# Performance work log

Measured on AMD Instinct MI355X. Metric: run time of the kernel, lower is better.

Reference implementation:

```python
import jax, jax.numpy as jnp
import numpy as np

B, L, D_INNER, D_STATE, DT_RANK, MODES = 4, 2048, 256, 16, 16, 32
LN_EPS = 1e-5


def setup_inputs() -> dict:
    key = jax.random.key(0)
    ks = jax.random.split(key, 10)
    x = jax.random.normal(ks[0], (B, L, D_INNER), dtype=jnp.float32)
    ln_g = jnp.ones((D_INNER,), jnp.float32)
    ln_b = jnp.zeros((D_INNER,), jnp.float32)
    W_xproj = jax.random.normal(ks[1], (DT_RANK + 2 * D_STATE, D_INNER), jnp.float32) * (D_INNER ** -0.5)
    dt_init_std = DT_RANK ** -0.5  # dt_scale = 1.0
    W_dt = jax.random.uniform(ks[2], (D_INNER, DT_RANK), jnp.float32, -dt_init_std, dt_init_std)
    dt = jnp.exp(jax.random.uniform(ks[3], (D_INNER,), jnp.float32) * (np.log(0.1) - np.log(0.001)) + np.log(0.001))
    dt = jnp.clip(dt, 1e-4, None)
    b_dt = dt + jnp.log(-jnp.expm1(-dt))  # inverse softplus
    A_log = jnp.zeros((D_INNER, D_STATE), jnp.float32)  # log(ones)
    D_param = jnp.ones((D_INNER,), jnp.float32)
    scale = 1.0 / (D_STATE * D_STATE)
    w_re = scale * jax.random.uniform(ks[4], (D_STATE, D_STATE, MODES), jnp.float32)
    w_im = scale * jax.random.uniform(ks[5], (D_STATE, D_STATE, MODES), jnp.float32)
    return {"x": x, "ln_g": ln_g, "ln_b": ln_b, "W_xproj": W_xproj, "W_dt": W_dt,
            "b_dt": b_dt, "A_log": A_log, "D_param": D_param, "w_re": w_re, "w_im": w_im}


def _fft_kernel(hs, w_re, w_im):
    # hs: (B, L, d_inner, d_state); rfft over d_inner with d_state channels
    h = jnp.transpose(hs, (0, 1, 3, 2))  # (B, L, k, N)
    hf = jnp.fft.rfft(h, axis=-1)        # (B, L, k, N//2+1) complex
    n_freq = D_INNER // 2 + 1
    l = min(MODES, n_freq)
    w = (w_re + 1j * w_im).astype(hf.dtype)
    of = jnp.einsum('blix,iox->blox', hf[..., :l], w[..., :l])
    of = jnp.pad(of, ((0, 0), (0, 0), (0, 0), (0, n_freq - l)))
    h2 = jnp.fft.irfft(of, n=D_INNER, axis=-1)  # real, (B, L, k, N)
    return jnp.transpose(h2, (0, 1, 3, 2))      # (B, L, d_inner, d_state)


def reference(x, ln_g, ln_b, W_xproj, W_dt, b_dt, A_log, D_param, w_re, w_im):
    # LayerNorm
    mu = jnp.mean(x, axis=-1, keepdims=True)
    var = jnp.var(x, axis=-1, keepdims=True)
    xn = (x - mu) * jax.lax.rsqrt(var + LN_EPS) * ln_g + ln_b

    A = -jnp.exp(A_log)  # (d_inner, d_state)
    dbc = xn @ W_xproj.T  # (B, L, dt_rank + 2*d_state)
    delta_r = dbc[..., :DT_RANK]
    Bc = dbc[..., DT_RANK:DT_RANK + D_STATE]        # (B, L, d_state)
    Cc = dbc[..., DT_RANK + D_STATE:]               # (B, L, d_state)
    delta = jax.nn.softplus(delta_r @ W_dt.T + b_dt)  # (B, L, d_inner)

    deltaA = jnp.exp(delta[..., None] * A)                       # (B, L, d_inner, d_state)
    BX = delta[..., None] * Bc[:, :, None, :] * xn[..., None]    # (B, L, d_inner, d_state)

    # selective scan: h_t = deltaA_t * h_{t-1} + BX_t (parallel associative scan over L)
    def comb(c1, c2):
        a1, b1 = c1
        a2, b2 = c2
        return a1 * a2, a2 * b1 + b2
    _, hs = jax.lax.associative_scan(comb, (deltaA, BX), axis=1)

    hs = _fft_kernel(hs, w_re, w_im)
    y = jnp.einsum('bldn,bln->bld', hs, Cc)  # hs @ C
    y = y + D_param * xn
    return y + x
```

## Files before the change

### kernel.cpp

```cpp
#include <hip/hip_runtime.h>
#include <hip/hip_bf16.h>

#define B_   4
#define L_   2048
#define D_   256
#define NC   128
#define CL   16
#define NBLK (B_*NC)
#define ANG  0.02454369260617025967f

typedef __bf16 bf16x8 __attribute__((ext_vector_type(8)));
typedef __bf16 bf16x4 __attribute__((ext_vector_type(4)));
typedef float  f32x4  __attribute__((ext_vector_type(4)));

__global__ __launch_bounds__(256) void k_lnscan(
        const float* __restrict__ x, const float* __restrict__ ln_g, const float* __restrict__ ln_b,
        const float* __restrict__ W_xproj, const float* __restrict__ W_dt,
        const float* __restrict__ b_dt, const float* __restrict__ A_log,
        unsigned int* __restrict__ dxn,
        float* __restrict__ Bc_o, float* __restrict__ Cc_o,
        float* __restrict__ dsum_o, float* __restrict__ S)
{
    __shared__ __align__(16) float xn_s[16 * 260];
    __shared__ __align__(16) __bf16 xnb[16 * 256];
    __shared__ float dbc_s[16 * 52];
    int tid = threadIdx.x, wave = tid >> 6, lane = tid & 63;
    int blk = blockIdx.x;
    int grow0 = blk * CL;
    char* xnb_c = (char*)xnb;

#pragma unroll
    for (int rr = 0; rr < 4; rr++) {
        int r = wave * 4 + rr;
        const float* xr = x + (size_t)(grow0 + r) * D_;
        float v[4];
#pragma unroll
        for (int q = 0; q < 4; q++) v[q] = xr[lane + q * 64];
        float sum = v[0] + v[1] + v[2] + v[3];
        float sq  = v[0]*v[0] + v[1]*v[1] + v[2]*v[2] + v[3]*v[3];
#pragma unroll
        for (int off = 32; off; off >>= 1) { sum += __shfl_xor(sum, off); sq += __shfl_xor(sq, off); }
        float mu = sum * (1.f / D_);
        float rstd = rsqrtf(sq * (1.f / D_) - mu * mu + 1e-5f);
#pragma unroll
        for (int q = 0; q < 4; q++) {
            int d = lane + q * 64;
            float xv = (v[q] - mu) * rstd * ln_g[d] + ln_b[d];
            xn_s[r * 260 + d] = xv;
            *(__bf16*)(xnb_c + r * 512 + ((d * 2) ^ ((r & 7) << 4))) = (__bf16)xv;
        }
    }
    __syncthreads();

    if (wave < 3) {
        int jcol = wave * 16 + (lane & 15);
        const float* wrow = W_xproj + (size_t)jcol * 256 + ((lane >> 4) * 8);
        int mrow = lane & 15;
        f32x4 acc = {0.f, 0.f, 0.f, 0.f};
#pragma unroll
        for (int ks = 0; ks < 8; ks++) {
            bf16x8 af = *(const bf16x8*)(xnb_c + mrow * 512 +
                          ((ks * 64 + ((lane >> 4) * 16)) ^ ((mrow & 7) << 4)));
            f32x4 wa = *(const f32x4*)(wrow + ks * 32);
            f32x4 wb = *(const f32x4*)(wrow + ks * 32 + 4);
            bf16x8 bf;
#pragma unroll
            for (int k = 0; k < 4; k++) { bf[k] = (__bf16)wa[k]; bf[4 + k] = (__bf16)wb[k]; }
            acc = __builtin_amdgcn_mfma_f32_16x16x32_bf16(af, bf, acc, 0, 0, 0);
        }
#pragma unroll
        for (int q = 0; q < 4; q++) {
            int r = (lane >> 4) * 4 + q;
            dbc_s[r * 52 + jcol] = acc[q];
            if (jcol >= 32)      Cc_o[(size_t)(grow0 + r) * 16 + jcol - 32] = acc[q];
            else if (jcol >= 16) Bc_o[(size_t)(grow0 + r) * 16 + jcol - 16] = acc[q];
        }
    }
    __syncthreads();

    int d = tid;
    float wdt[16];
#pragma unroll
    for (int q = 0; q < 4; q++) {
        f32x4 w4 = *(const f32x4*)&W_dt[d * 16 + q * 4];
#pragma unroll
        for (int k = 0; k < 4; k++) wdt[q * 4 + k] = w4[k];
    }
    float bd = b_dt[d];
    float dlt_r[16];
#pragma unroll
    for (int r = 0; r < 16; r++) {
        float din = bd;
#pragma unroll
        for (int k = 0; k < 16; k++) din = fmaf(dbc_s[r * 52 + k], wdt[k], din);
        din = (din > 15.f) ? din : log1pf(__expf(din));
        dlt_r[r] = din;
        union { __bf16 h2[2]; unsigned int u; } pk;
        pk.h2[0] = (__bf16)din;
        pk.h2[1] = (__bf16)xn_s[r * 260 + d];
        dxn[(size_t)(grow0 + r) * D_ + d] = pk.u;
    }

    float ar[16];
#pragma unroll
    for (int q = 0; q < 4; q++) {
        f32x4 a4 = *(const f32x4*)&A_log[d * 16 + q * 4];
#pragma unroll
        for (int k = 0; k < 4; k++) ar[q * 4 + k] = -__expf(a4[k]);
    }
    bool uni = true;
#pragma unroll
    for (int n = 1; n < 16; n++) uni = uni && (ar[n] == ar[0]);
    float s[16], dsum = 0.f;
#pragma unroll
    for (int n = 0; n < 16; n++) s[n] = 0.f;
    if (uni) {
        float ar0 = ar[0];
#pragma unroll
        for (int t = 0; t < CL; t++) {
            float dl = dlt_r[t];
            float dx = dl * xn_s[t * 260 + d];
            dsum += dl;
            float e = __expf(dl * ar0);
#pragma unroll
            for (int n = 0; n < 16; n++)
                s[n] = fmaf(e, s[n], dx * dbc_s[t * 52 + 16 + n]);
        }
    } else {
#pragma unroll
        for (int t = 0; t < CL; t++) {
            float dl = dlt_r[t];
            float dx = dl * xn_s[t * 260 + d];
            dsum += dl;
#pragma unroll
            for (int n = 0; n < 16; n++) {
                float e = __expf(dl * ar[n]);
                s[n] = fmaf(e, s[n], dx * dbc_s[t * 52 + 16 + n]);
            }
        }
    }
    dsum_o[(size_t)blk * 256 + d] = dsum;
    size_t o = (size_t)blk * 4096 + d * 16;
#pragma unroll
    for (int q = 0; q < 4; q++) {
        f32x4 sv;
#pragma unroll
        for (int k = 0; k < 4; k++) sv[k] = s[q*4+k];
        *reinterpret_cast<f32x4*>(&S[o + q * 4]) = sv;
    }
}

__global__ __launch_bounds__(256) void k_scan_tab(
        const float* __restrict__ A_log, const float* __restrict__ dsum,
        float* __restrict__ S_H0,
        const float* __restrict__ w_re, const float* __restrict__ w_im,
        __hip_bfloat16* __restrict__ E_t, __hip_bfloat16* __restrict__ wfrag,
        __hip_bfloat16* __restrict__ E_inv)
{
    int blk = blockIdx.x;
    if (blk >= NBLK) {
        int idx = (blk - NBLK) * 256 + threadIdx.x;
        if (idx < 16384) {
            int x = idx >> 8, d = idx & 255;
            float v = (x < 32) ? __cosf(ANG * (float)((x * d) & 255))
                               : -__sinf(ANG * (float)(((x - 32) * d) & 255));
            E_t[idx] = __float2bfloat16(v);
        } else if (idx < 49152) {
            int f = idx - 16384;
            int nt = f >> 9, l = (f >> 3) & 63, j = f & 7;
            int n = nt * 16 + (l & 15);
            int o = ((l >> 4) & 3) * 8 + j;
            float v = 0.f;
            if (o < 16) {
                int comp = n >> 9, xm = (n >> 4) & 31, i = n & 15;
                v = comp ? w_im[(i * 16 + o) * 32 + xm] : w_re[(i * 16 + o) * 32 + xm];
            }
            wfrag[f] = __float2bfloat16(v);
        } else {
            int f = idx - 49152;
            int nt = f >> 10, ks = (f >> 9) & 1, l = (f >> 3) & 63, j = f & 7;
            int row = ks * 32 + ((l >> 4) & 3) * 8 + j;
            int col = nt * 16 + (l & 15);
            float v = (row < 32) ? __cosf(ANG * (float)((row * col) & 255))
                                 : -__sinf(ANG * (float)(((row - 32) * col) & 255));
            E_inv[f] = __float2bfloat16(v);
        }
        return;
    }
    __shared__ float gP[256];
    __shared__ float gS[256];
    int tid = threadIdx.x;
    int g2 = tid >> 5, cl2 = tid & 31;
    int ch = blk * 32 + cl2;
    int b2 = ch >> 12, dn2 = ch & 4095;
    int dd = dn2 >> 4;
    float arv = -__expf(A_log[dn2]);
    size_t cb = ((size_t)b2 * NC + g2 * 16) * 4096 + dn2;
    size_t db = ((size_t)b2 * NC + g2 * 16) * 256 + dd;
    float pv[16], sv[16];
#pragma unroll
    for (int c = 0; c < 16; c++) {
        pv[c] = __expf(arv * dsum[db + (size_t)c * 256]);
        sv[c] = S_H0[cb + (size_t)c * 4096];
    }
    float pA = 1.f, sA = 0.f;
#pragma unroll
    for (int c = 0; c < 16; c++) { sA = fmaf(pv[c], sA, sv[c]); pA *= pv[c]; }
    gP[g2 * 32 + cl2] = pA;
    gS[g2 * 32 + cl2] = sA;
    __syncthreads();
    float h = 0.f;
    for (int gg = 0; gg < g2; gg++)
        h = fmaf(gP[gg * 32 + cl2], h, gS[gg * 32 + cl2]);
#pragma unroll
    for (int c = 0; c < 16; c++) {
        S_H0[cb + (size_t)c * 4096] = h;
        h = fmaf(pv[c], h, sv[c]);
    }
}

__global__ __launch_bounds__(256, 2) void k_fused(
        const unsigned int* __restrict__ dxn,
        const float* __restrict__ xin, const float* __restrict__ D_param,
        const float* __restrict__ Bc, const float* __restrict__ Cc,
        const float* __restrict__ A_log, const float* __restrict__ H0,
        float* __restrict__ out,
        const __hip_bfloat16* __restrict__ E_t, const __hip_bfloat16* __restrict__ wfrag,
        const __hip_bfloat16* __restrict__ E_inv)
{
    __shared__ __align__(16) char smem[69760];
    __bf16* hfb  = (__bf16*)(smem + 32768);
    __bf16* gsb  = (__bf16*)(smem + 65536);
    __bf16* ccb  = (__bf16*)(smem + 67712);
    float*  bc_s = (float*)(smem + 68736);

    int tid = threadIdx.x, wave = tid >> 6, lane = tid & 63;
    int wm = wave >> 1, wx = wave & 1;
    int blk = blockIdx.x;
    int grow0 = blk * CL;
    int d = tid;

    bc_s[tid] = Bc[(size_t)grow0 * 16 + tid];
    {
        float ccv = Cc[(size_t)grow0 * 16 + tid];
        int r = tid >> 4, o = tid & 15;
        ccb[r * 32 + o] = (__bf16)ccv;
        ccb[r * 32 + 16 + o] = (__bf16)0.f;
    }
    unsigned int dxnv[16];
#pragma unroll
    for (int t = 0; t < 16; t++) dxnv[t] = dxn[(size_t)(grow0 + t) * D_ + d];
    float ar[16], h[16];
    {
        size_t ho = (size_t)blk * 4096 + d * 16;
#pragma unroll
        for (int q = 0; q < 4; q++) {
            f32x4 a4 = *(const f32x4*)&A_log[d * 16 + q * 4];
            f32x4 h4 = *(const f32x4*)&H0[ho + q * 4];
#pragma unroll
            for (int k = 0; k < 4; k++) { ar[q*4+k] = -__expf(a4[k]); h[q*4+k] = h4[k]; }
        }
    }
    bool uni = true;
#pragma unroll
    for (int n = 1; n < 16; n++) uni = uni && (ar[n] == ar[0]);
    float ar0 = ar[0];

    bf16x8 bfragAll[2][8];
#pragma unroll
    for (int nt2 = 0; nt2 < 2; nt2++) {
        int xa = wx * 32 + nt2 * 16 + (lane & 15);
#pragma unroll
        for (int ks = 0; ks < 8; ks++)
            bfragAll[nt2][ks] = *(const bf16x8*)(E_t + xa * 256 + ks * 32 + ((lane >> 4) * 8));
    }
    int swz = (lane & 7) << 4;
    f32x4 acc[2][2];
#pragma unroll
    for (int a = 0; a < 2; a++)
#pragma unroll
        for (int b = 0; b < 2; b++) { acc[a][b][0]=0.f; acc[a][b][1]=0.f; acc[a][b][2]=0.f; acc[a][b][3]=0.f; }
    __syncthreads();

#pragma unroll
    for (int g = 0; g < 4; g++) {
        if (uni) {
#pragma unroll
            for (int tl = 0; tl < 4; tl++) {
                unsigned int v = dxnv[g * 4 + tl];
                float dl = __uint_as_float(v << 16);
                float dx = dl * __uint_as_float(v & 0xffff0000u);
                float e = __expf(dl * ar0);
#pragma unroll
                for (int n = 0; n < 16; n++) {
                    h[n] = fmaf(e, h[n], dx * bc_s[(g * 4 + tl) * 16 + n]);
                    int m = tl * 16 + n;
                    *(__bf16*)(smem + m * 512 + ((d * 2) ^ ((m & 7) << 4))) = (__bf16)h[n];
                }
            }
        } else {
#pragma unroll
            for (int tl = 0; tl < 4; tl++) {
                unsigned int v = dxnv[g * 4 + tl];
                float dl = __uint_as_float(v << 16);
                float dx = dl * __uint_as_float(v & 0xffff0000u);
#pragma unroll
                for (int n = 0; n < 16; n++) {
                    float e = __expf(dl * ar[n]);
                    h[n] = fmaf(e, h[n], dx * bc_s[(g * 4 + tl) * 16 + n]);
                    int m = tl * 16 + n;
                    *(__bf16*)(smem + m * 512 + ((d * 2) ^ ((m & 7) << 4))) = (__bf16)h[n];
                }
            }
        }
        __syncthreads();
#pragma unroll
        for (int ks = 0; ks < 8; ks++) {
#pragma unroll
            for (int tl2 = 0; tl2 < 2; tl2++) {
                int m = (wm * 2 + tl2) * 16 + (lane & 15);
                bf16x8 af = *(const bf16x8*)(smem + m * 512 + ((ks * 64 + ((lane >> 4) * 16)) ^ swz));
#pragma unroll
                for (int nt2 = 0; nt2 < 2; nt2++)
                    acc[tl2][nt2] = __builtin_amdgcn_mfma_f32_16x16x32_bf16(af, bfragAll[nt2][ks], acc[tl2][nt2], 0, 0, 0);
            }
        }
#pragma unroll
        for (int tl2 = 0; tl2 < 2; tl2++) {
            int r = g * 4 + wm * 2 + tl2;
#pragma unroll
            for (int nt2 = 0; nt2 < 2; nt2++) {
                int xcol = wx * 32 + nt2 * 16 + (lane & 15);
                bf16x4 pk;
#pragma unroll
                for (int k = 0; k < 4; k++) { pk[k] = (__bf16)acc[tl2][nt2][k]; acc[tl2][nt2][k] = 0.f; }
                *(bf16x4*)(&hfb[r * 1024 + xcol * 16 + (lane >> 4) * 4]) = pk;
            }
        }
        __syncthreads();
    }

    float xpf[4][4], xnpf[4][4], dpf[4];
#pragma unroll
    for (int ntl = 0; ntl < 4; ntl++) {
        int dcol = (wave * 4 + ntl) * 16 + (lane & 15);
        dpf[ntl] = D_param[dcol];
#pragma unroll
        for (int q = 0; q < 4; q++) {
            int r = (lane >> 4) * 4 + q;
            size_t go = (size_t)(grow0 + r) * D_ + dcol;
            xpf[ntl][q] = xin[go];
            xnpf[ntl][q] = __uint_as_float(dxn[go] & 0xffff0000u);
        }
    }

    {
        bf16x8 ccf = *(const bf16x8*)((char*)ccb + (lane & 15) * 64 + ((lane >> 4) * 16));
#pragma unroll
        for (int ntl = 0; ntl < 16; ntl++) {
            int nt = wave * 16 + ntl;
            f32x4 a = {0.f, 0.f, 0.f, 0.f};
            bf16x8 wf = *(const bf16x8*)(wfrag + (nt * 64 + lane) * 8);
            a = __builtin_amdgcn_mfma_f32_16x16x32_bf16(ccf, wf, a, 0, 0, 0);
            int col = nt * 16 + (lane & 15);
#pragma unroll
            for (int q = 0; q < 4; q++) {
                int r = (lane >> 4) * 4 + q;
                *(__bf16*)(smem + r * 2048 + col * 2) = (__bf16)a[q];
            }
        }
    }
    __syncthreads();

    {
        __bf16* wcb = (__bf16*)smem;
        int r = tid >> 4, x2 = tid & 15;
#pragma unroll
        for (int xh = 0; xh < 2; xh++) {
            int xs = xh * 16 + x2;
            bf16x8 hra = *(const bf16x8*)(&hfb[r * 1024 + xs * 16]);
            bf16x8 hrb = *(const bf16x8*)(&hfb[r * 1024 + xs * 16 + 8]);
            bf16x8 hia = *(const bf16x8*)(&hfb[r * 1024 + (xs + 32) * 16]);
            bf16x8 hib = *(const bf16x8*)(&hfb[r * 1024 + (xs + 32) * 16 + 8]);
            bf16x8 wra = *(const bf16x8*)(&wcb[r * 1024 + xs * 16]);
            bf16x8 wrb = *(const bf16x8*)(&wcb[r * 1024 + xs * 16 + 8]);
            bf16x8 wia = *(const bf16x8*)(&wcb[r * 1024 + 512 + xs * 16]);
            bf16x8 wib = *(const bf16x8*)(&wcb[r * 1024 + 512 + xs * 16 + 8]);
            float gre = 0.f, gim = 0.f;
#pragma unroll
            for (int k = 0; k < 8; k++) {
                float hr = (float)hra[k], hi = (float)hia[k];
                float wr = (float)wra[k], wi = (float)wia[k];
                gre = fmaf(hr, wr, gre); gre = fmaf(-hi, wi, gre);
                gim = fmaf(hr, wi, gim); gim = fmaf(hi, wr, gim);
                float hr2 = (float)hrb[k], hi2 = (float)hib[k];
                float wr2 = (float)wrb[k], wi2 = (float)wib[k];
                gre = fmaf(hr2, wr2, gre); gre = fmaf(-hi2, wi2, gre);
                gim = fmaf(hr2, wi2, gim); gim = fmaf(hi2, wr2, gim);
            }
            float sc = xs ? 2.f : 1.f;
            gsb[r * 68 + xs]      = (__bf16)(gre * sc);
            gsb[r * 68 + 32 + xs] = (__bf16)(gim * sc);
        }
    }
    __syncthreads();

    {
        bf16x8 ga0 = *(const bf16x8*)((char*)gsb + (lane & 15) * 136 + ((lane >> 4) * 16));
        bf16x8 ga1 = *(const bf16x8*)((char*)gsb + (lane & 15) * 136 + 64 + ((lane >> 4) * 16));
#pragma unroll
        for (int ntl = 0; ntl < 4; ntl++) {
            int nt = wave * 4 + ntl;
            f32x4 a = {0.f, 0.f, 0.f, 0.f};
            a = __builtin_amdgcn_mfma_f32_16x16x32_bf16(
                    ga0, *(const bf16x8*)(E_inv + ((nt * 2 + 0) * 64 + lane) * 8), a, 0, 0, 0);
            a = __builtin_amdgcn_mfma_f32_16x16x32_bf16(
                    ga1, *(const bf16x8*)(E_inv + ((nt * 2 + 1) * 64 + lane) * 8), a, 0, 0, 0);
            int dcol = nt * 16 + (lane & 15);
#pragma unroll
            for (int q = 0; q < 4; q++) {
                int r = (lane >> 4) * 4 + q;
                size_t go = (size_t)(grow0 + r) * D_ + dcol;
                out[go] = xpf[ntl][q] + dpf[ntl] * xnpf[ntl][q] + a[q] * (1.f / 256.f);
            }
        }
    }
}

extern "C" void kernel_launch(void* const* d_in, const int* in_sizes, int n_in,
                              void* d_out, int out_size, void* d_ws, size_t ws_size,
                              hipStream_t stream)
{
    const float* x       = (const float*)d_in[0];
    const float* ln_g    = (const float*)d_in[1];
    const float* ln_b    = (const float*)d_in[2];
    const float* W_xproj = (const float*)d_in[3];
    const float* W_dt    = (const float*)d_in[4];
    const float* b_dt    = (const float*)d_in[5];
    const float* A_log   = (const float*)d_in[6];
    const float* D_param = (const float*)d_in[7];
    const float* w_re    = (const float*)d_in[8];
    const float* w_im    = (const float*)d_in[9];

    float* ws    = (float*)d_ws;
    float* S_H0  = ws;
    unsigned int* dxn = (unsigned int*)(S_H0 + 2097152);
    float* Bc    = (float*)(dxn + 2097152);
    float* Cc    = Bc + 131072;
    float* dsum  = Cc + 131072;
    __hip_bfloat16* tab = (__hip_bfloat16*)(dsum + 131072);
    __hip_bfloat16* E_t   = tab;
    __hip_bfloat16* wfrag = tab + 16384;
    __hip_bfloat16* E_inv = tab + 49152;
    float* out = (float*)d_out;

    hipLaunchKernelGGL(k_lnscan, dim3(NBLK), dim3(256), 0, stream,
                       x, ln_g, ln_b, W_xproj, W_dt, b_dt, A_log,
                       dxn, Bc, Cc, dsum, S_H0);
    hipLaunchKernelGGL(k_scan_tab, dim3(NBLK + 256), dim3(256), 0, stream,
                       A_log, dsum, S_H0, w_re, w_im, E_t, wfrag, E_inv);
    hipLaunchKernelGGL(k_fused, dim3(NBLK), dim3(256), 0, stream,
                       dxn, x, D_param, Bc, Cc, A_log, S_H0, out, E_t, wfrag, E_inv);
}
```

Measured before the change: 50.93 us.

## Split each fused chunk into two half-blocks to double grid and occupancy

The fused scan+FFT kernel now launches two blocks per 16-row chunk. Each block handles 8 output rows, and the second half first replays the scan over the first 8 timesteps to recover its starting state. Shared memory is roughly halved and launch bounds are raised to 4 blocks per CU, which exposes more parallelism and lets more waves hide latency. The cost is the redundant scan recomputation in the second half, duplicated loads of dxn and the tables, and half-empty MFMA tiles in the C-projection and inverse-FFT stages.

```diff
diff --git a/kernel.cpp b/kernel.cpp
--- a/kernel.cpp
+++ b/kernel.cpp
@@ -219,7 +219,7 @@
     }
 }
 
-__global__ __launch_bounds__(256, 2) void k_fused(
+__global__ __launch_bounds__(256, 4) void k_fused(
         const unsigned int* __restrict__ dxn,
         const float* __restrict__ xin, const float* __restrict__ D_param,
         const float* __restrict__ Bc, const float* __restrict__ Cc,
@@ -228,31 +228,32 @@
         const __hip_bfloat16* __restrict__ E_t, const __hip_bfloat16* __restrict__ wfrag,
         const __hip_bfloat16* __restrict__ E_inv)
 {
-    __shared__ __align__(16) char smem[69760];
-    __bf16* hfb  = (__bf16*)(smem + 32768);
-    __bf16* gsb  = (__bf16*)(smem + 65536);
-    __bf16* ccb  = (__bf16*)(smem + 67712);
-    float*  bc_s = (float*)(smem + 68736);
+    __shared__ __align__(16) char smem[36992];
+    __bf16* hfb  = (__bf16*)(smem + 16384);
+    __bf16* gsb  = (__bf16*)(smem + 32768);
+    __bf16* ccb  = (__bf16*)(smem + 34944);
+    float*  bc_s = (float*)(smem + 35968);
 
     int tid = threadIdx.x, wave = tid >> 6, lane = tid & 63;
-    int wm = wave >> 1, wx = wave & 1;
-    int blk = blockIdx.x;
-    int grow0 = blk * CL;
+    int mt = wave & 1, nx = wave >> 1;
+    int chunk = blockIdx.x & 511, half = blockIdx.x >> 9;
+    int grow0c = chunk * CL;
+    int row_base = grow0c + half * 8;
     int d = tid;
 
-    bc_s[tid] = Bc[(size_t)grow0 * 16 + tid];
-    {
-        float ccv = Cc[(size_t)grow0 * 16 + tid];
+    bc_s[tid] = Bc[(size_t)grow0c * 16 + tid];
+    if (tid < 128) {
         int r = tid >> 4, o = tid & 15;
+        float ccv = Cc[(size_t)(row_base + r) * 16 + o];
         ccb[r * 32 + o] = (__bf16)ccv;
         ccb[r * 32 + 16 + o] = (__bf16)0.f;
     }
     unsigned int dxnv[16];
 #pragma unroll
-    for (int t = 0; t < 16; t++) dxnv[t] = dxn[(size_t)(grow0 + t) * D_ + d];
+    for (int t = 0; t < 16; t++) dxnv[t] = dxn[(size_t)(grow0c + t) * D_ + d];
     float ar[16], h[16];
     {
-        size_t ho = (size_t)blk * 4096 + d * 16;
+        size_t ho = (size_t)chunk * 4096 + d * 16;
 #pragma unroll
         for (int q = 0; q < 4; q++) {
             f32x4 a4 = *(const f32x4*)&A_log[d * 16 + q * 4];
@@ -269,45 +270,65 @@
     bf16x8 bfragAll[2][8];
 #pragma unroll
     for (int nt2 = 0; nt2 < 2; nt2++) {
-        int xa = wx * 32 + nt2 * 16 + (lane & 15);
+        int xa = nx * 32 + nt2 * 16 + (lane & 15);
 #pragma unroll
         for (int ks = 0; ks < 8; ks++)
             bfragAll[nt2][ks] = *(const bf16x8*)(E_t + xa * 256 + ks * 32 + ((lane >> 4) * 8));
     }
     int swz = (lane & 7) << 4;
-    f32x4 acc[2][2];
-#pragma unroll
-    for (int a = 0; a < 2; a++)
-#pragma unroll
-        for (int b = 0; b < 2; b++) { acc[a][b][0]=0.f; acc[a][b][1]=0.f; acc[a][b][2]=0.f; acc[a][b][3]=0.f; }
-    __syncthreads();
-
-#pragma unroll
-    for (int g = 0; g < 4; g++) {
+    f32x4 acc[2];
+#pragma unroll
+    for (int b = 0; b < 2; b++) { acc[b][0]=0.f; acc[b][1]=0.f; acc[b][2]=0.f; acc[b][3]=0.f; }
+
+    if (half) {
         if (uni) {
 #pragma unroll
-            for (int tl = 0; tl < 4; tl++) {
-                unsigned int v = dxnv[g * 4 + tl];
+            for (int t = 0; t < 8; t++) {
+                unsigned int v = dxnv[t];
                 float dl = __uint_as_float(v << 16);
                 float dx = dl * __uint_as_float(v & 0xffff0000u);
                 float e = __expf(dl * ar0);
 #pragma unroll
+                for (int n = 0; n < 16; n++)
+                    h[n] = fmaf(e, h[n], dx * bc_s[t * 16 + n]);
+            }
+        } else {
+#pragma unroll
+            for (int t = 0; t < 8; t++) {
+                unsigned int v = dxnv[t];
+                float dl = __uint_as_float(v << 16);
+                float dx = dl * __uint_as_float(v & 0xffff0000u);
+#pragma unroll
                 for (int n = 0; n < 16; n++) {
-                    h[n] = fmaf(e, h[n], dx * bc_s[(g * 4 + tl) * 16 + n]);
+                    float e = __expf(dl * ar[n]);
+                    h[n] = fmaf(e, h[n], dx * bc_s[t * 16 + n]);
+                }
+            }
+        }
+    }
+    __syncthreads();
+
+#pragma unroll
+    for (int g = 0; g < 4; g++) {
+#pragma unroll
+        for (int tl = 0; tl < 2; tl++) {
+            int t = half * 8 + g * 2 + tl;
+            unsigned int v = dxnv[t];
+            float dl = __uint_as_float(v << 16);
+            float dx = dl * __uint_as_float(v & 0xffff0000u);
+            if (uni) {
+                float e = __expf(dl * ar0);
+#pragma unroll
+                for (int n = 0; n < 16; n++) {
+                    h[n] = fmaf(e, h[n], dx * bc_s[t * 16 + n]);
                     int m = tl * 16 + n;
                     *(__bf16*)(smem + m * 512 + ((d * 2) ^ ((m & 7) << 4))) = (__bf16)h[n];
                 }
-            }
-        } else {
-#pragma unroll
-            for (int tl = 0; tl < 4; tl++) {
-                unsigned int v = dxnv[g * 4 + tl];
-                float dl = __uint_as_float(v << 16);
-                float dx = dl * __uint_as_float(v & 0xffff0000u);
+            } else {
 #pragma unroll
                 for (int n = 0; n < 16; n++) {
                     float e = __expf(dl * ar[n]);
-                    h[n] = fmaf(e, h[n], dx * bc_s[(g * 4 + tl) * 16 + n]);
+                    h[n] = fmaf(e, h[n], dx * bc_s[t * 16 + n]);
                     int m = tl * 16 + n;
                     *(__bf16*)(smem + m * 512 + ((d * 2) ^ ((m & 7) << 4))) = (__bf16)h[n];
                 }
@@ -316,24 +337,20 @@
         __syncthreads();
 #pragma unroll
         for (int ks = 0; ks < 8; ks++) {
-#pragma unroll
-            for (int tl2 = 0; tl2 < 2; tl2++) {
-                int m = (wm * 2 + tl2) * 16 + (lane & 15);
-                bf16x8 af = *(const bf16x8*)(smem + m * 512 + ((ks * 64 + ((lane >> 4) * 16)) ^ swz));
-#pragma unroll
-                for (int nt2 = 0; nt2 < 2; nt2++)
-                    acc[tl2][nt2] = __builtin_amdgcn_mfma_f32_16x16x32_bf16(af, bfragAll[nt2][ks], acc[tl2][nt2], 0, 0, 0);
-            }
-        }
-#pragma unroll
-        for (int tl2 = 0; tl2 < 2; tl2++) {
-            int r = g * 4 + wm * 2 + tl2;
+            int m = mt * 16 + (lane & 15);
+            bf16x8 af = *(const bf16x8*)(smem + m * 512 + ((ks * 64 + ((lane >> 4) * 16)) ^ swz));
+#pragma unroll
+            for (int nt2 = 0; nt2 < 2; nt2++)
+                acc[nt2] = __builtin_amdgcn_mfma_f32_16x16x32_bf16(af, bfragAll[nt2][ks], acc[nt2], 0, 0, 0);
+        }
+        {
+            int r = g * 2 + mt;
 #pragma unroll
             for (int nt2 = 0; nt2 < 2; nt2++) {
-                int xcol = wx * 32 + nt2 * 16 + (lane & 15);
+                int xcol = nx * 32 + nt2 * 16 + (lane & 15);
                 bf16x4 pk;
 #pragma unroll
-                for (int k = 0; k < 4; k++) { pk[k] = (__bf16)acc[tl2][nt2][k]; acc[tl2][nt2][k] = 0.f; }
+                for (int k = 0; k < 4; k++) { pk[k] = (__bf16)acc[nt2][k]; acc[nt2][k] = 0.f; }
                 *(bf16x4*)(&hfb[r * 1024 + xcol * 16 + (lane >> 4) * 4]) = pk;
             }
         }
@@ -348,9 +365,11 @@
 #pragma unroll
         for (int q = 0; q < 4; q++) {
             int r = (lane >> 4) * 4 + q;
-            size_t go = (size_t)(grow0 + r) * D_ + dcol;
-            xpf[ntl][q] = xin[go];
-            xnpf[ntl][q] = __uint_as_float(dxn[go] & 0xffff0000u);
+            if (r < 8) {
+                size_t go = (size_t)(row_base + r) * D_ + dcol;
+                xpf[ntl][q] = xin[go];
+                xnpf[ntl][q] = __uint_as_float(dxn[go] & 0xffff0000u);
+            } else { xpf[ntl][q] = 0.f; xnpf[ntl][q] = 0.f; }
         }
     }
 
@@ -366,7 +385,7 @@
 #pragma unroll
             for (int q = 0; q < 4; q++) {
                 int r = (lane >> 4) * 4 + q;
-                *(__bf16*)(smem + r * 2048 + col * 2) = (__bf16)a[q];
+                if (r < 8) *(__bf16*)(smem + r * 2048 + col * 2) = (__bf16)a[q];
             }
         }
     }
@@ -374,34 +393,30 @@
 
     {
         __bf16* wcb = (__bf16*)smem;
-        int r = tid >> 4, x2 = tid & 15;
-#pragma unroll
-        for (int xh = 0; xh < 2; xh++) {
-            int xs = xh * 16 + x2;
-            bf16x8 hra = *(const bf16x8*)(&hfb[r * 1024 + xs * 16]);
-            bf16x8 hrb = *(const bf16x8*)(&hfb[r * 1024 + xs * 16 + 8]);
-            bf16x8 hia = *(const bf16x8*)(&hfb[r * 1024 + (xs + 32) * 16]);
-            bf16x8 hib = *(const bf16x8*)(&hfb[r * 1024 + (xs + 32) * 16 + 8]);
-            bf16x8 wra = *(const bf16x8*)(&wcb[r * 1024 + xs * 16]);
-            bf16x8 wrb = *(const bf16x8*)(&wcb[r * 1024 + xs * 16 + 8]);
-            bf16x8 wia = *(const bf16x8*)(&wcb[r * 1024 + 512 + xs * 16]);
-            bf16x8 wib = *(const bf16x8*)(&wcb[r * 1024 + 512 + xs * 16 + 8]);
-            float gre = 0.f, gim = 0.f;
-#pragma unroll
-            for (int k = 0; k < 8; k++) {
-                float hr = (float)hra[k], hi = (float)hia[k];
-                float wr = (float)wra[k], wi = (float)wia[k];
-                gre = fmaf(hr, wr, gre); gre = fmaf(-hi, wi, gre);
-                gim = fmaf(hr, wi, gim); gim = fmaf(hi, wr, gim);
-                float hr2 = (float)hrb[k], hi2 = (float)hib[k];
-                float wr2 = (float)wrb[k], wi2 = (float)wib[k];
-                gre = fmaf(hr2, wr2, gre); gre = fmaf(-hi2, wi2, gre);
-                gim = fmaf(hr2, wi2, gim); gim = fmaf(hi2, wr2, gim);
-            }
-            float sc = xs ? 2.f : 1.f;
-            gsb[r * 68 + xs]      = (__bf16)(gre * sc);
-            gsb[r * 68 + 32 + xs] = (__bf16)(gim * sc);
-        }
+        int r = tid >> 5, xs = tid & 31;
+        bf16x8 hra = *(const bf16x8*)(&hfb[r * 1024 + xs * 16]);
+        bf16x8 hrb = *(const bf16x8*)(&hfb[r * 1024 + xs * 16 + 8]);
+        bf16x8 hia = *(const bf16x8*)(&hfb[r * 1024 + (xs + 32) * 16]);
+        bf16x8 hib = *(const bf16x8*)(&hfb[r * 1024 + (xs + 32) * 16 + 8]);
+        bf16x8 wra = *(const bf16x8*)(&wcb[r * 1024 + xs * 16]);
+        bf16x8 wrb = *(const bf16x8*)(&wcb[r * 1024 + xs * 16 + 8]);
+        bf16x8 wia = *(const bf16x8*)(&wcb[r * 1024 + 512 + xs * 16]);
+        bf16x8 wib = *(const bf16x8*)(&wcb[r * 1024 + 512 + xs * 16 + 8]);
+        float gre = 0.f, gim = 0.f;
+#pragma unroll
+        for (int k = 0; k < 8; k++) {
+            float hr = (float)hra[k], hi = (float)hia[k];
+            float wr = (float)wra[k], wi = (float)wia[k];
+            gre = fmaf(hr, wr, gre); gre = fmaf(-hi, wi, gre);
+            gim = fmaf(hr, wi, gim); gim = fmaf(hi, wr, gim);
+            float hr2 = (float)hrb[k], hi2 = (float)hib[k];
+            float wr2 = (float)wrb[k], wi2 = (float)wib[k];
+            gre = fmaf(hr2, wr2, gre); gre = fmaf(-hi2, wi2, gre);
+            gim = fmaf(hr2, wi2, gim); gim = fmaf(hi2, wr2, gim);
+        }
+        float sc = xs ? 2.f : 1.f;
+        gsb[r * 68 + xs]      = (__bf16)(gre * sc);
+        gsb[r * 68 + 32 + xs] = (__bf16)(gim * sc);
     }
     __syncthreads();
 
@@ -420,8 +435,10 @@
 #pragma unroll
             for (int q = 0; q < 4; q++) {
                 int r = (lane >> 4) * 4 + q;
-                size_t go = (size_t)(grow0 + r) * D_ + dcol;
-                out[go] = xpf[ntl][q] + dpf[ntl] * xnpf[ntl][q] + a[q] * (1.f / 256.f);
+                if (r < 8) {
+                    size_t go = (size_t)(row_base + r) * D_ + dcol;
+                    out[go] = xpf[ntl][q] + dpf[ntl] * xnpf[ntl][q] + a[q] * (1.f / 256.f);
+                }
             }
         }
     }
@@ -459,6 +476,6 @@
                        dxn, Bc, Cc, dsum, S_H0);
     hipLaunchKernelGGL(k_scan_tab, dim3(NBLK + 256), dim3(256), 0, stream,
                        A_log, dsum, S_H0, w_re, w_im, E_t, wfrag, E_inv);
-    hipLaunchKernelGGL(k_fused, dim3(NBLK), dim3(256), 0, stream,
+    hipLaunchKernelGGL(k_fused, dim3(2 * NBLK), dim3(256), 0, stream,
                        dxn, x, D_param, Bc, Cc, A_log, S_H0, out, E_t, wfrag, E_inv);
 }
```

After: 86.30 us. 69.4% more time.

## Shrink k_fused shared memory to fit three blocks per CU

Applied to the files above, without the earlier changes.

Cuts k_fused's LDS footprint from about 68KB to about 52KB so three blocks fit per CU, and raises launch bounds to match. The scan now stages 2 timesteps per group (8 groups instead of 4), and each wave computes one 16-row MFMA tile instead of two. The frequency-weight product is split into real and imaginary passes that reuse a half-size buffer, with an extra barrier per pass. The intent is more occupancy to hide latency, at the cost of twice as many barriers in the scan loop and tighter register limits that may cause spills.

```diff
diff --git a/kernel.cpp b/kernel.cpp
--- a/kernel.cpp
+++ b/kernel.cpp
@@ -219,7 +219,7 @@
     }
 }
 
-__global__ __launch_bounds__(256, 2) void k_fused(
+__global__ __launch_bounds__(256, 3) void k_fused(
         const unsigned int* __restrict__ dxn,
         const float* __restrict__ xin, const float* __restrict__ D_param,
         const float* __restrict__ Bc, const float* __restrict__ Cc,
@@ -228,14 +228,14 @@
         const __hip_bfloat16* __restrict__ E_t, const __hip_bfloat16* __restrict__ wfrag,
         const __hip_bfloat16* __restrict__ E_inv)
 {
-    __shared__ __align__(16) char smem[69760];
-    __bf16* hfb  = (__bf16*)(smem + 32768);
-    __bf16* gsb  = (__bf16*)(smem + 65536);
-    __bf16* ccb  = (__bf16*)(smem + 67712);
-    float*  bc_s = (float*)(smem + 68736);
+    __shared__ __align__(16) char smem[53376];
+    __bf16* hfb  = (__bf16*)(smem + 16384);
+    __bf16* gsb  = (__bf16*)(smem + 49152);
+    __bf16* ccb  = (__bf16*)(smem + 51328);
+    float*  bc_s = (float*)(smem + 52352);
 
     int tid = threadIdx.x, wave = tid >> 6, lane = tid & 63;
-    int wm = wave >> 1, wx = wave & 1;
+    int mt = wave & 1, nx = wave >> 1;
     int blk = blockIdx.x;
     int grow0 = blk * CL;
     int d = tid;
@@ -269,45 +269,38 @@
     bf16x8 bfragAll[2][8];
 #pragma unroll
     for (int nt2 = 0; nt2 < 2; nt2++) {
-        int xa = wx * 32 + nt2 * 16 + (lane & 15);
+        int xa = nx * 32 + nt2 * 16 + (lane & 15);
 #pragma unroll
         for (int ks = 0; ks < 8; ks++)
             bfragAll[nt2][ks] = *(const bf16x8*)(E_t + xa * 256 + ks * 32 + ((lane >> 4) * 8));
     }
     int swz = (lane & 7) << 4;
-    f32x4 acc[2][2];
-#pragma unroll
-    for (int a = 0; a < 2; a++)
-#pragma unroll
-        for (int b = 0; b < 2; b++) { acc[a][b][0]=0.f; acc[a][b][1]=0.f; acc[a][b][2]=0.f; acc[a][b][3]=0.f; }
+    f32x4 acc[2];
+#pragma unroll
+    for (int b = 0; b < 2; b++) { acc[b][0]=0.f; acc[b][1]=0.f; acc[b][2]=0.f; acc[b][3]=0.f; }
     __syncthreads();
 
 #pragma unroll
-    for (int g = 0; g < 4; g++) {
-        if (uni) {
-#pragma unroll
-            for (int tl = 0; tl < 4; tl++) {
-                unsigned int v = dxnv[g * 4 + tl];
-                float dl = __uint_as_float(v << 16);
-                float dx = dl * __uint_as_float(v & 0xffff0000u);
+    for (int g = 0; g < 8; g++) {
+#pragma unroll
+        for (int tl = 0; tl < 2; tl++) {
+            int t = g * 2 + tl;
+            unsigned int v = dxnv[t];
+            float dl = __uint_as_float(v << 16);
+            float dx = dl * __uint_as_float(v & 0xffff0000u);
+            if (uni) {
                 float e = __expf(dl * ar0);
 #pragma unroll
                 for (int n = 0; n < 16; n++) {
-                    h[n] = fmaf(e, h[n], dx * bc_s[(g * 4 + tl) * 16 + n]);
+                    h[n] = fmaf(e, h[n], dx * bc_s[t * 16 + n]);
                     int m = tl * 16 + n;
                     *(__bf16*)(smem + m * 512 + ((d * 2) ^ ((m & 7) << 4))) = (__bf16)h[n];
                 }
-            }
-        } else {
-#pragma unroll
-            for (int tl = 0; tl < 4; tl++) {
-                unsigned int v = dxnv[g * 4 + tl];
-                float dl = __uint_as_float(v << 16);
-                float dx = dl * __uint_as_float(v & 0xffff0000u);
+            } else {
 #pragma unroll
                 for (int n = 0; n < 16; n++) {
                     float e = __expf(dl * ar[n]);
-                    h[n] = fmaf(e, h[n], dx * bc_s[(g * 4 + tl) * 16 + n]);
+                    h[n] = fmaf(e, h[n], dx * bc_s[t * 16 + n]);
                     int m = tl * 16 + n;
                     *(__bf16*)(smem + m * 512 + ((d * 2) ^ ((m & 7) << 4))) = (__bf16)h[n];
                 }
@@ -316,24 +309,20 @@
         __syncthreads();
 #pragma unroll
         for (int ks = 0; ks < 8; ks++) {
-#pragma unroll
-            for (int tl2 = 0; tl2 < 2; tl2++) {
-                int m = (wm * 2 + tl2) * 16 + (lane & 15);
-                bf16x8 af = *(const bf16x8*)(smem + m * 512 + ((ks * 64 + ((lane >> 4) * 16)) ^ swz));
-#pragma unroll
-                for (int nt2 = 0; nt2 < 2; nt2++)
-                    acc[tl2][nt2] = __builtin_amdgcn_mfma_f32_16x16x32_bf16(af, bfragAll[nt2][ks], acc[tl2][nt2], 0, 0, 0);
-            }
-        }
-#pragma unroll
-        for (int tl2 = 0; tl2 < 2; tl2++) {
-            int r = g * 4 + wm * 2 + tl2;
+            int m = mt * 16 + (lane & 15);
+            bf16x8 af = *(const bf16x8*)(smem + m * 512 + ((ks * 64 + ((lane >> 4) * 16)) ^ swz));
+#pragma unroll
+            for (int nt2 = 0; nt2 < 2; nt2++)
+                acc[nt2] = __builtin_amdgcn_mfma_f32_16x16x32_bf16(af, bfragAll[nt2][ks], acc[nt2], 0, 0, 0);
+        }
+        {
+            int r = g * 2 + mt;
 #pragma unroll
             for (int nt2 = 0; nt2 < 2; nt2++) {
-                int xcol = wx * 32 + nt2 * 16 + (lane & 15);
+                int xcol = nx * 32 + nt2 * 16 + (lane & 15);
                 bf16x4 pk;
 #pragma unroll
-                for (int k = 0; k < 4; k++) { pk[k] = (__bf16)acc[tl2][nt2][k]; acc[tl2][nt2][k] = 0.f; }
+                for (int k = 0; k < 4; k++) { pk[k] = (__bf16)acc[nt2][k]; acc[nt2][k] = 0.f; }
                 *(bf16x4*)(&hfb[r * 1024 + xcol * 16 + (lane >> 4) * 4]) = pk;
             }
         }
@@ -354,54 +343,55 @@
         }
     }
 
-    {
-        bf16x8 ccf = *(const bf16x8*)((char*)ccb + (lane & 15) * 64 + ((lane >> 4) * 16));
-#pragma unroll
-        for (int ntl = 0; ntl < 16; ntl++) {
-            int nt = wave * 16 + ntl;
+    float gre[2], gim[2];
+    gre[0] = gre[1] = gim[0] = gim[1] = 0.f;
+    bf16x8 ccf = *(const bf16x8*)((char*)ccb + (lane & 15) * 64 + ((lane >> 4) * 16));
+    int gr = tid >> 4, gx2 = tid & 15;
+#pragma unroll
+    for (int comp = 0; comp < 2; comp++) {
+#pragma unroll
+        for (int ntl = 0; ntl < 8; ntl++) {
+            int nt = comp * 32 + wave * 8 + ntl;
             f32x4 a = {0.f, 0.f, 0.f, 0.f};
             bf16x8 wf = *(const bf16x8*)(wfrag + (nt * 64 + lane) * 8);
             a = __builtin_amdgcn_mfma_f32_16x16x32_bf16(ccf, wf, a, 0, 0, 0);
-            int col = nt * 16 + (lane & 15);
+            int coln = (nt - comp * 32) * 16 + (lane & 15);
 #pragma unroll
             for (int q = 0; q < 4; q++) {
                 int r = (lane >> 4) * 4 + q;
-                *(__bf16*)(smem + r * 2048 + col * 2) = (__bf16)a[q];
-            }
-        }
-    }
-    __syncthreads();
-
-    {
+                *(__bf16*)(smem + r * 1024 + coln * 2) = (__bf16)a[q];
+            }
+        }
+        __syncthreads();
         __bf16* wcb = (__bf16*)smem;
-        int r = tid >> 4, x2 = tid & 15;
 #pragma unroll
         for (int xh = 0; xh < 2; xh++) {
-            int xs = xh * 16 + x2;
-            bf16x8 hra = *(const bf16x8*)(&hfb[r * 1024 + xs * 16]);
-            bf16x8 hrb = *(const bf16x8*)(&hfb[r * 1024 + xs * 16 + 8]);
-            bf16x8 hia = *(const bf16x8*)(&hfb[r * 1024 + (xs + 32) * 16]);
-            bf16x8 hib = *(const bf16x8*)(&hfb[r * 1024 + (xs + 32) * 16 + 8]);
-            bf16x8 wra = *(const bf16x8*)(&wcb[r * 1024 + xs * 16]);
-            bf16x8 wrb = *(const bf16x8*)(&wcb[r * 1024 + xs * 16 + 8]);
-            bf16x8 wia = *(const bf16x8*)(&wcb[r * 1024 + 512 + xs * 16]);
-            bf16x8 wib = *(const bf16x8*)(&wcb[r * 1024 + 512 + xs * 16 + 8]);
-            float gre = 0.f, gim = 0.f;
+            int xs = xh * 16 + gx2;
+            bf16x8 hra = *(const bf16x8*)(&hfb[gr * 1024 + xs * 16]);
+            bf16x8 hrb = *(const bf16x8*)(&hfb[gr * 1024 + xs * 16 + 8]);
+            bf16x8 hia = *(const bf16x8*)(&hfb[gr * 1024 + (xs + 32) * 16]);
+            bf16x8 hib = *(const bf16x8*)(&hfb[gr * 1024 + (xs + 32) * 16 + 8]);
+            bf16x8 wva = *(const bf16x8*)(&wcb[gr * 512 + xs * 16]);
+            bf16x8 wvb = *(const bf16x8*)(&wcb[gr * 512 + xs * 16 + 8]);
+            float sre = 0.f, sim = 0.f;
 #pragma unroll
             for (int k = 0; k < 8; k++) {
-                float hr = (float)hra[k], hi = (float)hia[k];
-                float wr = (float)wra[k], wi = (float)wia[k];
-                gre = fmaf(hr, wr, gre); gre = fmaf(-hi, wi, gre);
-                gim = fmaf(hr, wi, gim); gim = fmaf(hi, wr, gim);
-                float hr2 = (float)hrb[k], hi2 = (float)hib[k];
-                float wr2 = (float)wrb[k], wi2 = (float)wib[k];
-                gre = fmaf(hr2, wr2, gre); gre = fmaf(-hi2, wi2, gre);
-                gim = fmaf(hr2, wi2, gim); gim = fmaf(hi2, wr2, gim);
-            }
-            float sc = xs ? 2.f : 1.f;
-            gsb[r * 68 + xs]      = (__bf16)(gre * sc);
-            gsb[r * 68 + 32 + xs] = (__bf16)(gim * sc);
-        }
+                float hr = (float)hra[k], hi = (float)hia[k], wv = (float)wva[k];
+                sre = fmaf(hr, wv, sre); sim = fmaf(hi, wv, sim);
+                float hr2 = (float)hrb[k], hi2 = (float)hib[k], wv2 = (float)wvb[k];
+                sre = fmaf(hr2, wv2, sre); sim = fmaf(hi2, wv2, sim);
+            }
+            if (comp == 0) { gre[xh] += sre; gim[xh] += sim; }
+            else           { gre[xh] -= sim; gim[xh] += sre; }
+        }
+        __syncthreads();
+    }
+#pragma unroll
+    for (int xh = 0; xh < 2; xh++) {
+        int xs = xh * 16 + gx2;
+        float sc = xs ? 2.f : 1.f;
+        gsb[gr * 68 + xs]      = (__bf16)(gre[xh] * sc);
+        gsb[gr * 68 + 32 + xs] = (__bf16)(gim[xh] * sc);
     }
     __syncthreads();
 
```

Result: slower. 52.79 us (+3.6%).
